# Kernel optimization log

Hardware: AMD Instinct MI355X
Metric: run time of the kernel (lower is better)

## Reference

```python
import jax, jax.numpy as jnp
import numpy as np

B, T, C = 16, 512, 32
W = 128            # max_window
SERIES_LEN = 100000
WIN_MIN, WIN_MAX = 2.0, 64.0
SHARP = 1.0        # fixed sharpness of the soft window edge
BN_EPS = 1e-5


def setup_inputs() -> dict:
    key = jax.random.key(0)
    ks = jax.random.split(key, 6)
    x = jax.random.normal(ks[0], (B, T, C), jnp.float32)
    full_series = jax.random.normal(ks[1], (SERIES_LEN, C), jnp.float32)
    # starts >= W so the lookback window never needs padding; end = start + T
    starts = jax.random.randint(ks[2], (B,), W, SERIES_LEN - T)
    indices = jnp.stack([starts, starts + T], axis=1).astype(jnp.int32)  # (B, 2)
    # raw (logit-space) per-channel window sizes, as in the torch init
    raw_win_mean = jax.random.normal(ks[3], (C,), jnp.float32)
    raw_win_std = jax.random.normal(ks[4], (C,), jnp.float32)
    return dict(
        x=x, full_series=full_series, indices=indices,
        raw_win_mean=raw_win_mean, raw_win_std=raw_win_std,
        gamma_mean=jnp.ones((C,), jnp.float32), beta_mean=jnp.zeros((C,), jnp.float32),
        gamma_std=jnp.ones((C,), jnp.float32), beta_std=jnp.zeros((C,), jnp.float32),
    )


def _soft_window_weights(raw_win):
    # sigmoid-mapped window size in [WIN_MIN, WIN_MAX], per channel
    win = WIN_MIN + jax.nn.sigmoid(raw_win) * (WIN_MAX - WIN_MIN)          # (C,)
    age = jnp.arange(W, dtype=jnp.float32)[::-1]                            # slot W-1 is most recent (age 0)
    w = jax.nn.sigmoid(SHARP * (win[None, :] - age[:, None]))               # (W, C)
    return w


def _rolling_windows(full_series, starts):
    # batch_windows[b] = full_series[starts[b]-W : starts[b]+T]   -> (B, W+T, C)
    offs = jnp.arange(W + T)
    bw = full_series[(starts - W)[:, None] + offs[None, :]]                 # (B, W+T, C)
    # window for output step t covers slots [t, t+W) (the W points before the current step)
    tidx = jnp.arange(T)[:, None] + jnp.arange(W)[None, :]                  # (T, W)
    return bw[:, tidx, :]                                                   # (B, T, W, C)


def _batchnorm(f, gamma, beta):
    # BatchNorm1d over (B, C, T): normalize per channel over batch and time, biased var
    mean = f.mean(axis=(0, 1))
    var = ((f - mean) ** 2).mean(axis=(0, 1))
    return (f - mean) * jax.lax.rsqrt(var + BN_EPS) * gamma + beta


def reference(x, full_series, indices, raw_win_mean, raw_win_std,
              gamma_mean, beta_mean, gamma_std, beta_std):
    starts = indices[:, 0]
    xw = _rolling_windows(full_series, starts)                              # (B, T, W, C)

    # feature 1: soft-window weighted mean
    w1 = _soft_window_weights(raw_win_mean)                                 # (W, C)
    s1 = jnp.sum(w1, axis=0)                                                # (C,)
    f_mean = jnp.einsum('btwc,wc->btc', xw, w1) / s1                        # (B, T, C)

    # feature 2: soft-window weighted std
    w2 = _soft_window_weights(raw_win_std)
    s2 = jnp.sum(w2, axis=0)
    m2 = jnp.einsum('btwc,wc->btc', xw, w2) / s2
    var2 = jnp.einsum('btwc,wc->btc', (xw - m2[:, :, None, :]) ** 2, w2) / s2
    f_std = jnp.sqrt(var2 + 1e-8)

    out_mean = _batchnorm(f_mean, gamma_mean, beta_mean)
    out_std = _batchnorm(f_std, gamma_std, beta_std)
    return jnp.concatenate([x, out_mean, out_std], axis=-1)                 # (B, T, 3*C)
```

## Files before the change

### kernel.cpp

```cpp
#include <hip/hip_runtime.h>
#include <math.h>

#define NB 16
#define NT 512
#define NC 32
#define NW 128
#define TILE_T 32
#define NTILES (NT / TILE_T)
#define NBLK (NB * NTILES)
#define NROWS (TILE_T + NW)
#define XS 36
#define WIN_MIN_F 2.0f
#define WIN_RANGE_F 62.0f
#define EINV_F 0.36787944117f

#define WS_FMEAN 0
#define WS_FSTD  (NB*NT*NC)
#define WS_PART  (2*NB*NT*NC)

typedef float v2f __attribute__((ext_vector_type(2)));

__device__ __forceinline__ float fast_sigmoid_neg(float a) {
    return __builtin_amdgcn_rcpf(1.0f + __expf(a));
}
__device__ __forceinline__ v2f pk_fma(v2f a, v2f b, v2f c) {
    return __builtin_elementwise_fma(a, b, c);
}

#define U_M    0
#define U_SWH  3072
#define U_RED  3200

__global__ __launch_bounds__(256) void feat_main(
    const float* __restrict__ x,
    const float* __restrict__ series,
    const int*   __restrict__ indices,
    const float* __restrict__ rwm,
    const float* __restrict__ rws,
    float* __restrict__ f_mean,
    float* __restrict__ f_std,
    float* __restrict__ partials,
    float* __restrict__ out)
{
    __shared__ __align__(16) float s_x[NROWS * XS];
    __shared__ __align__(16) float s_u[NW * 64];
    __shared__ float s_win[2 * NC];

    const int tid = threadIdx.x;
    const int blk = blockIdx.x;
    const int b   = blk >> 4;
    const int tt  = blk & 15;
    const int t0  = tt * TILE_T;
    const int start = indices[2 * b];

    {
        const int row = b * NT + t0 + (tid >> 3);
        const int q = tid & 7;
        ((float4*)out)[row * 24 + q] = ((const float4*)x)[row * 8 + q];
    }

    if (tid < 2 * NC) {
        const float raw = (tid < NC) ? rwm[tid] : rws[tid - NC];
        s_win[tid] = WIN_MIN_F + WIN_RANGE_F * fast_sigmoid_neg(-raw);
    }

    const float4* src4 = (const float4*)(series + (size_t)(start - NW + t0) * NC);
#pragma unroll
    for (int k = 0; k < 5; ++k) {
        const int j = tid + k * 256;
        const int row = j >> 3, c4 = (j & 7) << 2;
        *(float4*)&s_x[row * XS + c4] = src4[j];
    }
    __syncthreads();

    {
        const int c  = tid & 31;
        const int wc = tid >> 5;
        const int w0t = wc * 16;
        const float age0 = (float)(NW - 1 - w0t);
        float E1 = __expf(age0 - s_win[c]);
        float E2 = __expf(age0 - s_win[NC + c]);
#pragma unroll
        for (int j = 0; j < 16; ++j) {
            const int base = (w0t + j) * 64 + (c >> 1) * 4 + (c & 1);
            s_u[base]     = __builtin_amdgcn_rcpf(1.0f + E1);
            s_u[base + 2] = __builtin_amdgcn_rcpf(1.0f + E2);
            E1 *= EINV_F;
            E2 *= EINV_F;
        }
    }
    __syncthreads();

    const int cp   = tid & 15;
    const int tg   = tid >> 4;
    const int half = tg >> 3;
    const int rg   = tg & 7;
    const int r0   = rg * 4;
    const int base = r0 + half * 64;

    const v2f*    xv2 = (const v2f*)s_x;
    const float4* wv4 = (const float4*)s_u;

    v2f a1[4], a2[4], a3[4];
#pragma unroll
    for (int k = 0; k < 4; ++k) { a1[k] = (v2f){0.f,0.f}; a2[k] = (v2f){0.f,0.f}; a3[k] = (v2f){0.f,0.f}; }
    v2f sw1 = {0.f,0.f}, sw2 = {0.f,0.f};

    v2f xs[4], qs[4];
#pragma unroll
    for (int k = 0; k < 4; ++k) {
        xs[k] = xv2[(base + k) * 18 + cp];
        qs[k] = xs[k] * xs[k];
    }

    const int w0 = half * 64;
#pragma unroll 4
    for (int i = 0; i < 64; ++i) {
        const float4 wv = wv4[(w0 + i) * 16 + cp];
        const v2f wlo = {wv.x, wv.y};
        const v2f whi = {wv.z, wv.w};
        sw1 = sw1 + wlo;
        sw2 = sw2 + whi;
#pragma unroll
        for (int k = 0; k < 4; ++k) {
            a1[k] = pk_fma(xs[k], wlo, a1[k]);
            a2[k] = pk_fma(xs[k], whi, a2[k]);
            a3[k] = pk_fma(qs[k], whi, a3[k]);
        }
        const v2f xn = xv2[(base + i + 4) * 18 + cp];
        xs[0] = xs[1]; qs[0] = qs[1];
        xs[1] = xs[2]; qs[1] = qs[2];
        xs[2] = xs[3]; qs[2] = qs[3];
        xs[3] = xn;    qs[3] = xn * xn;
    }

    __syncthreads();

    v2f* s_m   = (v2f*)&s_u[U_M];
    v2f* s_swh = (v2f*)&s_u[U_SWH];
    v2f* s_red = (v2f*)&s_u[U_RED];

    if (half) {
        v2f* m = &s_m[(rg * 16 + cp) * 12];
#pragma unroll
        for (int k = 0; k < 4; ++k) {
            m[k]     = a1[k];
            m[4 + k] = a2[k];
            m[8 + k] = a3[k];
        }
        if (rg == 0) {
            s_swh[cp * 2]     = sw1;
            s_swh[cp * 2 + 1] = sw2;
        }
    }
    __syncthreads();

    if (!half) {
        const v2f* m = &s_m[(rg * 16 + cp) * 12];
#pragma unroll
        for (int k = 0; k < 4; ++k) {
            a1[k] = a1[k] + m[k];
            a2[k] = a2[k] + m[4 + k];
            a3[k] = a3[k] + m[8 + k];
        }
        sw1 = sw1 + s_swh[cp * 2];
        sw2 = sw2 + s_swh[cp * 2 + 1];

        v2f inv1, inv2;
        inv1.x = __builtin_amdgcn_rcpf(sw1.x); inv1.y = __builtin_amdgcn_rcpf(sw1.y);
        inv2.x = __builtin_amdgcn_rcpf(sw2.x); inv2.y = __builtin_amdgcn_rcpf(sw2.y);

        v2f p0 = {0.f,0.f}, p1 = {0.f,0.f}, p2 = {0.f,0.f}, p3 = {0.f,0.f};
#pragma unroll
        for (int k = 0; k < 4; ++k) {
            const v2f fm = a1[k] * inv1;
            const v2f m2 = a2[k] * inv2;
            const v2f e2 = a3[k] * inv2;
            v2f fs;
            fs.x = sqrtf(fmaxf(e2.x - m2.x * m2.x, 0.f) + 1e-8f);
            fs.y = sqrtf(fmaxf(e2.y - m2.y * m2.y, 0.f) + 1e-8f);
            const size_t o2 = ((size_t)(b * NT + t0 + r0 + k)) * 16 + cp;
            ((v2f*)f_mean)[o2] = fm;
            ((v2f*)f_std)[o2]  = fs;
            p0 = p0 + fm;
            p1 = pk_fma(fm, fm, p1);
            p2 = p2 + fs;
            p3 = pk_fma(fs, fs, p3);
        }
        s_red[(0 * 8 + rg) * 16 + cp] = p0;
        s_red[(1 * 8 + rg) * 16 + cp] = p1;
        s_red[(2 * 8 + rg) * 16 + cp] = p2;
        s_red[(3 * 8 + rg) * 16 + cp] = p3;
    }
    __syncthreads();

    if (tid < 64) {
        const int stat = tid >> 4, cc = tid & 15;
        v2f s = {0.f, 0.f};
#pragma unroll
        for (int g = 0; g < 8; ++g)
            s = s + s_red[(stat * 8 + g) * 16 + cc];
        ((v2f*)partials)[blk * 64 + stat * 16 + cc] = s;
    }
}

__global__ __launch_bounds__(256) void bn_write(
    const float* __restrict__ f_mean,
    const float* __restrict__ f_std,
    const float* __restrict__ partials,
    const float* __restrict__ gm, const float* __restrict__ bm,
    const float* __restrict__ gs, const float* __restrict__ bs,
    float* __restrict__ out)
{
    __shared__ __align__(16) float s_part[8 * 128];
    __shared__ __align__(16) float s_sums[128];
    __shared__ __align__(16) float s_coef[4 * NC];

    const int tid = threadIdx.x;

    {
        const int cell  = tid & 31;
        const int slice = tid >> 5;
        const float4* p4 = (const float4*)partials;
        float4 acc = {0.f, 0.f, 0.f, 0.f};
#pragma unroll 8
        for (int i = 0; i < 32; ++i) {
            const float4 v = p4[(slice * 32 + i) * 32 + cell];
            acc.x += v.x; acc.y += v.y; acc.z += v.z; acc.w += v.w;
        }
        *(float4*)&s_part[(slice * 32 + cell) * 4] = acc;
    }
    __syncthreads();
    if (tid < 32) {
        float4 s = {0.f, 0.f, 0.f, 0.f};
#pragma unroll
        for (int sl = 0; sl < 8; ++sl) {
            const float4 v = ((const float4*)s_part)[sl * 32 + tid];
            s.x += v.x; s.y += v.y; s.z += v.z; s.w += v.w;
        }
        ((float4*)s_sums)[tid] = s;
    }
    __syncthreads();
    if (tid < NC) {
        const float invN = 1.0f / (float)(NB * NT);
        const float mu_m  = s_sums[tid] * invN;
        float var_m = s_sums[32 + tid] * invN - mu_m * mu_m;
        var_m = fmaxf(var_m, 0.0f);
        const float A1 = gm[tid] / sqrtf(var_m + 1e-5f);
        const float B1 = bm[tid] - mu_m * A1;
        const float mu_s  = s_sums[64 + tid] * invN;
        float var_s = s_sums[96 + tid] * invN - mu_s * mu_s;
        var_s = fmaxf(var_s, 0.0f);
        const float A2 = gs[tid] / sqrtf(var_s + 1e-5f);
        const float B2 = bs[tid] - mu_s * A2;
        s_coef[tid]          = A1;
        s_coef[NC + tid]     = B1;
        s_coef[2 * NC + tid] = A2;
        s_coef[3 * NC + tid] = B2;
    }
    __syncthreads();

    const float4* fm4 = (const float4*)f_mean;
    const float4* fs4 = (const float4*)f_std;
    const float4* cf4 = (const float4*)s_coef;
    float4* out4 = (float4*)out;
    const int row0 = blockIdx.x * 32;

#pragma unroll
    for (int k = 0; k < 2; ++k) {
        const int j = tid + k * 256;
        const int r = j >> 4;
        const int q = j & 15;
        const int row = row0 + r;
        float4 v;
        int oq;
        if (q < 8) {
            const float4 f = fm4[row * 8 + q];
            const float4 A = cf4[q], Bv = cf4[8 + q];
            v.x = fmaf(f.x, A.x, Bv.x); v.y = fmaf(f.y, A.y, Bv.y);
            v.z = fmaf(f.z, A.z, Bv.z); v.w = fmaf(f.w, A.w, Bv.w);
            oq = 8 + q;
        } else {
            const int m = q - 8;
            const float4 f = fs4[row * 8 + m];
            const float4 A = cf4[16 + m], Bv = cf4[24 + m];
            v.x = fmaf(f.x, A.x, Bv.x); v.y = fmaf(f.y, A.y, Bv.y);
            v.z = fmaf(f.z, A.z, Bv.z); v.w = fmaf(f.w, A.w, Bv.w);
            oq = 16 + m;
        }
        out4[row * 24 + oq] = v;
    }
}

extern "C" void kernel_launch(void* const* d_in, const int* in_sizes, int n_in,
                              void* d_out, int out_size, void* d_ws, size_t ws_size,
                              hipStream_t stream) {
    const float* x      = (const float*)d_in[0];
    const float* series = (const float*)d_in[1];
    const int*   idx    = (const int*)d_in[2];
    const float* rwm    = (const float*)d_in[3];
    const float* rws    = (const float*)d_in[4];
    const float* gm     = (const float*)d_in[5];
    const float* bm     = (const float*)d_in[6];
    const float* gs     = (const float*)d_in[7];
    const float* bs     = (const float*)d_in[8];
    float* out = (float*)d_out;
    float* ws  = (float*)d_ws;

    float* f_mean   = ws + WS_FMEAN;
    float* f_std    = ws + WS_FSTD;
    float* partials = ws + WS_PART;

    feat_main<<<NBLK, 256, 0, stream>>>(x, series, idx, rwm, rws, f_mean, f_std, partials, out);
    bn_write<<<NBLK, 256, 0, stream>>>(f_mean, f_std, partials, gm, bm, gs, bs, out);
}
```

Baseline: 15.70 us.

## Split window reduction four ways across 512 threads with wavefront shuffle combine

Doubles the feat_main block to 512 threads and splits the 128-wide window into four 32-slot quarters per row group instead of two halves. The partial sums are combined with xor shuffles inside the 64-lane wavefront, which replaces the shared-memory partial exchange and two barriers. This shortens each thread's serial FMA loop and adds latency hiding on a grid of only 256 blocks. In exchange it adds shuffle instructions, uses more threads per block, and leaves most threads idle in the epilogue.

```diff
diff --git a/kernel.cpp b/kernel.cpp
--- a/kernel.cpp
+++ b/kernel.cpp
@@ -27,11 +27,7 @@
     return __builtin_elementwise_fma(a, b, c);
 }
 
-#define U_M    0
-#define U_SWH  3072
-#define U_RED  3200
-
-__global__ __launch_bounds__(256) void feat_main(
+__global__ __launch_bounds__(512) void feat_main(
     const float* __restrict__ x,
     const float* __restrict__ series,
     const int*   __restrict__ indices,
@@ -45,6 +41,7 @@
     __shared__ __align__(16) float s_x[NROWS * XS];
     __shared__ __align__(16) float s_u[NW * 64];
     __shared__ float s_win[2 * NC];
+    __shared__ __align__(16) float s_red[4 * 8 * NC];
 
     const int tid = threadIdx.x;
     const int blk = blockIdx.x;
@@ -53,7 +50,7 @@
     const int t0  = tt * TILE_T;
     const int start = indices[2 * b];
 
-    {
+    if (tid < 256) {
         const int row = b * NT + t0 + (tid >> 3);
         const int q = tid & 7;
         ((float4*)out)[row * 24 + q] = ((const float4*)x)[row * 8 + q];
@@ -66,22 +63,24 @@
 
     const float4* src4 = (const float4*)(series + (size_t)(start - NW + t0) * NC);
 #pragma unroll
-    for (int k = 0; k < 5; ++k) {
-        const int j = tid + k * 256;
-        const int row = j >> 3, c4 = (j & 7) << 2;
-        *(float4*)&s_x[row * XS + c4] = src4[j];
+    for (int k = 0; k < 3; ++k) {
+        const int j = tid + k * 512;
+        if (j < NROWS * 8) {
+            const int row = j >> 3, c4 = (j & 7) << 2;
+            *(float4*)&s_x[row * XS + c4] = src4[j];
+        }
     }
     __syncthreads();
 
     {
-        const int c  = tid & 31;
-        const int wc = tid >> 5;
-        const int w0t = wc * 16;
+        const int c   = tid & 31;
+        const int wc  = tid >> 5;
+        const int w0t = wc * 8;
         const float age0 = (float)(NW - 1 - w0t);
         float E1 = __expf(age0 - s_win[c]);
         float E2 = __expf(age0 - s_win[NC + c]);
 #pragma unroll
-        for (int j = 0; j < 16; ++j) {
+        for (int j = 0; j < 8; ++j) {
             const int base = (w0t + j) * 64 + (c >> 1) * 4 + (c & 1);
             s_u[base]     = __builtin_amdgcn_rcpf(1.0f + E1);
             s_u[base + 2] = __builtin_amdgcn_rcpf(1.0f + E2);
@@ -91,12 +90,12 @@
     }
     __syncthreads();
 
-    const int cp   = tid & 15;
-    const int tg   = tid >> 4;
-    const int half = tg >> 3;
-    const int rg   = tg & 7;
-    const int r0   = rg * 4;
-    const int base = r0 + half * 64;
+    const int rg = tid >> 6;
+    const int qr = (tid >> 4) & 3;
+    const int cp = tid & 15;
+    const int r0 = rg * 4;
+    const int w0 = qr * 32;
+    const int base = r0 + w0;
 
     const v2f*    xv2 = (const v2f*)s_x;
     const float4* wv4 = (const float4*)s_u;
@@ -113,9 +112,8 @@
         qs[k] = xs[k] * xs[k];
     }
 
-    const int w0 = half * 64;
 #pragma unroll 4
-    for (int i = 0; i < 64; ++i) {
+    for (int i = 0; i < 32; ++i) {
         const float4 wv = wv4[(w0 + i) * 16 + cp];
         const v2f wlo = {wv.x, wv.y};
         const v2f whi = {wv.z, wv.w};
@@ -134,38 +132,20 @@
         xs[3] = xn;    qs[3] = xn * xn;
     }
 
-    __syncthreads();
-
-    v2f* s_m   = (v2f*)&s_u[U_M];
-    v2f* s_swh = (v2f*)&s_u[U_SWH];
-    v2f* s_red = (v2f*)&s_u[U_RED];
-
-    if (half) {
-        v2f* m = &s_m[(rg * 16 + cp) * 12];
+#pragma unroll
+    for (int mask = 16; mask < 64; mask <<= 1) {
 #pragma unroll
         for (int k = 0; k < 4; ++k) {
-            m[k]     = a1[k];
-            m[4 + k] = a2[k];
-            m[8 + k] = a3[k];
-        }
-        if (rg == 0) {
-            s_swh[cp * 2]     = sw1;
-            s_swh[cp * 2 + 1] = sw2;
-        }
-    }
-    __syncthreads();
-
-    if (!half) {
-        const v2f* m = &s_m[(rg * 16 + cp) * 12];
-#pragma unroll
-        for (int k = 0; k < 4; ++k) {
-            a1[k] = a1[k] + m[k];
-            a2[k] = a2[k] + m[4 + k];
-            a3[k] = a3[k] + m[8 + k];
-        }
-        sw1 = sw1 + s_swh[cp * 2];
-        sw2 = sw2 + s_swh[cp * 2 + 1];
-
+            a1[k].x += __shfl_xor(a1[k].x, mask); a1[k].y += __shfl_xor(a1[k].y, mask);
+            a2[k].x += __shfl_xor(a2[k].x, mask); a2[k].y += __shfl_xor(a2[k].y, mask);
+            a3[k].x += __shfl_xor(a3[k].x, mask); a3[k].y += __shfl_xor(a3[k].y, mask);
+        }
+        sw1.x += __shfl_xor(sw1.x, mask); sw1.y += __shfl_xor(sw1.y, mask);
+        sw2.x += __shfl_xor(sw2.x, mask); sw2.y += __shfl_xor(sw2.y, mask);
+    }
+
+    v2f* s_redv = (v2f*)s_red;
+    if (qr == 0) {
         v2f inv1, inv2;
         inv1.x = __builtin_amdgcn_rcpf(sw1.x); inv1.y = __builtin_amdgcn_rcpf(sw1.y);
         inv2.x = __builtin_amdgcn_rcpf(sw2.x); inv2.y = __builtin_amdgcn_rcpf(sw2.y);
@@ -187,10 +167,10 @@
             p2 = p2 + fs;
             p3 = pk_fma(fs, fs, p3);
         }
-        s_red[(0 * 8 + rg) * 16 + cp] = p0;
-        s_red[(1 * 8 + rg) * 16 + cp] = p1;
-        s_red[(2 * 8 + rg) * 16 + cp] = p2;
-        s_red[(3 * 8 + rg) * 16 + cp] = p3;
+        s_redv[(0 * 8 + rg) * 16 + cp] = p0;
+        s_redv[(1 * 8 + rg) * 16 + cp] = p1;
+        s_redv[(2 * 8 + rg) * 16 + cp] = p2;
+        s_redv[(3 * 8 + rg) * 16 + cp] = p3;
     }
     __syncthreads();
 
@@ -199,7 +179,7 @@
         v2f s = {0.f, 0.f};
 #pragma unroll
         for (int g = 0; g < 8; ++g)
-            s = s + s_red[(stat * 8 + g) * 16 + cc];
+            s = s + s_redv[(stat * 8 + g) * 16 + cc];
         ((v2f*)partials)[blk * 64 + stat * 16 + cc] = s;
     }
 }
@@ -311,6 +291,6 @@
     float* f_std    = ws + WS_FSTD;
     float* partials = ws + WS_PART;
 
-    feat_main<<<NBLK, 256, 0, stream>>>(x, series, idx, rwm, rws, f_mean, f_std, partials, out);
+    feat_main<<<NBLK, 512, 0, stream>>>(x, series, idx, rwm, rws, f_mean, f_std, partials, out);
     bn_write<<<NBLK, 256, 0, stream>>>(f_mean, f_std, partials, gm, bm, gs, bs, out);
 }
```

Measured after the change: 16.70 us. 1.06x slower.
